# Kernel optimization log

Measured on AMD Instinct MI355X. Metric: run time of the kernel, lower is better.

## Reference

```python
import jax, jax.numpy as jnp
import numpy as np

N_NODES = 50000
N_EDGES = 640000
D = 128      # in_feats
OUT = 128    # out_feats


def setup_inputs() -> dict:
    key = jax.random.key(0)
    ks = jax.random.split(key, 8)
    feat = jax.random.normal(ks[0], (N_NODES, D), dtype=jnp.float32)
    weight = jax.random.uniform(ks[1], (N_EDGES,), dtype=jnp.float32)
    src = jax.random.randint(ks[2], (N_EDGES,), 0, N_NODES, dtype=jnp.int64)
    dst = jax.random.randint(ks[3], (N_EDGES,), 0, N_NODES, dtype=jnp.int64)
    # xavier_uniform with relu gain ~ sqrt(2)*sqrt(6/(fan_in+fan_out))
    g = np.sqrt(2.0)
    lim_pool = g * np.sqrt(6.0 / (D + D))
    lim_neigh = g * np.sqrt(6.0 / (2 * D + OUT))
    W_pool = jax.random.uniform(ks[4], (D, D), dtype=jnp.float32, minval=-lim_pool, maxval=lim_pool)
    b_pool = jnp.zeros((D,), dtype=jnp.float32)
    W_neigh = jax.random.uniform(ks[5], (OUT, 2 * D), dtype=jnp.float32, minval=-lim_neigh, maxval=lim_neigh)
    b_neigh = jnp.zeros((OUT,), dtype=jnp.float32)
    return {"feat": feat, "weight": weight, "src": src, "dst": dst,
            "W_pool": W_pool, "b_pool": b_pool, "W_neigh": W_neigh, "b_neigh": b_neigh}


def reference(feat, weight, src, dst, W_pool, b_pool, W_neigh, b_neigh):
    n = feat.shape[0]
    # fc_pool: h = feat @ W_pool.T + b_pool  -> [N, D]
    h = feat @ W_pool.T + b_pool
    # u_mul_e: per-edge message m_e = h[src_e] * w_e  -> [E, D]
    m = h[src] * weight[:, None]
    # max reduce over incoming edges (scatter-max by dst)
    neigh = jax.ops.segment_max(m, dst, num_segments=n)
    # zero-degree nodes get 0 (segment_max fills empties with -inf)
    deg = jax.ops.segment_sum(jnp.ones_like(weight), dst, num_segments=n)
    neigh = jnp.where(deg[:, None] > 0, neigh, jnp.zeros((), dtype=feat.dtype))
    # fc_neigh on concat(feat, neigh)
    rst = jnp.concatenate([feat, neigh], axis=1) @ W_neigh.T + b_neigh
    return rst
```

## Files before the change

### kernel.cpp

```cpp
#include <hip/hip_runtime.h>
#include <cstdint>
#include <cstddef>

#define N_NODES 50000
#define N_EDGES 640000
#define DF 128
#define SLOT 64

#define SC_BLOCKS 625
#define GEMM_BLOCKS 782
#define FRAG_BLOCKS 16

typedef __attribute__((ext_vector_type(8))) short bf16x8;
typedef __attribute__((ext_vector_type(4))) float f32x4;

__device__ inline unsigned short f2bf(float f) {
    unsigned int u = __float_as_uint(f);
    return (unsigned short)((u + 0x7fffu + ((u >> 16) & 1u)) >> 16);
}

__global__ __launch_bounds__(256) void k1_scatter_gemm(
    const float* __restrict__ feat,
    const float* __restrict__ W_pool,
    const float* __restrict__ W_neigh,
    const float* __restrict__ b_pool,
    const int* __restrict__ src,
    const int* __restrict__ dst,
    const float* __restrict__ w,
    unsigned short* __restrict__ featb,
    unsigned short* __restrict__ hb,
    unsigned short* __restrict__ Wn1_f,
    unsigned short* __restrict__ Wn2_f,
    int* __restrict__ cnt,
    uint2* __restrict__ edges)
{
    int bid = blockIdx.x;
    int t = threadIdx.x;
    if (bid < SC_BLOCKS) {
        int base = bid * 1024;
        #pragma unroll
        for (int k = 0; k < 4; ++k) {
            int e = base + k * 256 + t;
            int s = src[e], d = dst[e];
            float wv = w[e];
            int c = atomicAdd(&cnt[d], 1);
            if (c < SLOT) {
                uint2 r; r.x = (unsigned int)s; r.y = __float_as_uint(wv);
                edges[(size_t)d * SLOT + c] = r;
            }
        }
    } else if (bid < SC_BLOCKS + GEMM_BLOCKS) {
        __shared__ __align__(16) unsigned short wsh[16384];
        #pragma unroll
        for (int k = 0; k < 8; ++k) {
            int r8 = t * 8 + k;
            int L = r8 & 63, tt2 = (r8 >> 6) & 3, c = r8 >> 8;
            const float* srcp = W_pool + (c * 16 + (L & 15)) * 128
                                       + tt2 * 32 + (L >> 4) * 8;
            float4 a = ((const float4*)srcp)[0];
            float4 b = ((const float4*)srcp)[1];
            ushort4 lo, hi;
            lo.x = f2bf(a.x); lo.y = f2bf(a.y); lo.z = f2bf(a.z); lo.w = f2bf(a.w);
            hi.x = f2bf(b.x); hi.y = f2bf(b.y); hi.z = f2bf(b.z); hi.w = f2bf(b.w);
            ((ushort4*)(wsh + r8 * 8))[0] = lo;
            ((ushort4*)(wsh + r8 * 8))[1] = hi;
        }
        __syncthreads();

        int gwave = (bid - SC_BLOCKS) * 4 + (t >> 6);
        int m0 = gwave * 16;
        if (m0 < N_NODES) {
            int lane = t & 63;
            const int n = lane & 15, quad = lane >> 4;
            f32x4 acc[8];
            #pragma unroll
            for (int c = 0; c < 8; ++c) {
                float bv = b_pool[c * 16 + n];
                acc[c] = (f32x4){bv, bv, bv, bv};
            }
            const float* fp = feat + (size_t)(m0 + n) * DF + quad * 8;
            unsigned short* fbp = featb + (size_t)(m0 + n) * DF + quad * 8;
            #pragma unroll
            for (int tt = 0; tt < 4; ++tt) {
                float4 a = ((const float4*)(fp + tt * 32))[0];
                float4 b = ((const float4*)(fp + tt * 32))[1];
                union { bf16x8 v; ushort4 u4[2]; } af;
                af.u4[0].x = f2bf(a.x); af.u4[0].y = f2bf(a.y);
                af.u4[0].z = f2bf(a.z); af.u4[0].w = f2bf(a.w);
                af.u4[1].x = f2bf(b.x); af.u4[1].y = f2bf(b.y);
                af.u4[1].z = f2bf(b.z); af.u4[1].w = f2bf(b.w);
                *(bf16x8*)(fbp + tt * 32) = af.v;
                #pragma unroll
                for (int c = 0; c < 8; ++c) {
                    bf16x8 bfv = *(const bf16x8*)(wsh + (size_t)((c * 4 + tt) * 64 + lane) * 8);
                    acc[c] = __builtin_amdgcn_mfma_f32_16x16x32_bf16(af.v, bfv, acc[c], 0, 0, 0);
                }
            }
            #pragma unroll
            for (int c = 0; c < 8; ++c)
                #pragma unroll
                for (int r = 0; r < 4; ++r)
                    hb[(size_t)(m0 + quad * 4 + r) * DF + c * 16 + n] = f2bf(acc[c][r]);
        }
    } else {
        int g = (bid - SC_BLOCKS - GEMM_BLOCKS) * 256 + t;
        int m = g >> 11;
        int r8 = g & 2047;
        int L = r8 & 63, tt = (r8 >> 6) & 3, c = r8 >> 8;
        int o = c * 16 + (L & 15);
        int kb = tt * 32 + (L >> 4) * 8;
        const float* srcp = W_neigh + o * 256 + (m ? 128 : 0) + kb;
        unsigned short* dstp = m ? Wn2_f : Wn1_f;
        ushort4 lo, hi;
        float4 a = ((const float4*)srcp)[0];
        float4 b = ((const float4*)srcp)[1];
        lo.x = f2bf(a.x); lo.y = f2bf(a.y); lo.z = f2bf(a.z); lo.w = f2bf(a.w);
        hi.x = f2bf(b.x); hi.y = f2bf(b.y); hi.z = f2bf(b.z); hi.w = f2bf(b.w);
        ((ushort4*)(dstp + r8 * 8))[0] = lo;
        ((ushort4*)(dstp + r8 * 8))[1] = hi;
    }
}

__global__ __launch_bounds__(256) void neigh_max_kernel(
    const unsigned short* __restrict__ hb,
    const int* __restrict__ cnt,
    const uint2* __restrict__ edges,
    unsigned short* __restrict__ neighb)
{
    int gwave = (blockIdx.x * 256 + threadIdx.x) >> 6;
    if (gwave >= N_NODES) return;
    int node = __builtin_amdgcn_readfirstlane(gwave);
    int lane = threadIdx.x & 63;
    const int half = lane >> 5;
    const int q = lane & 31;

    int beg = node * SLOT;
    int dg = cnt[node]; if (dg > SLOT) dg = SLOT;
    int end = beg + dg;
    float4 acc = make_float4(-3.4e38f, -3.4e38f, -3.4e38f, -3.4e38f);

    for (int e = beg; e < end; e += 8) {
        int i1 = min(e + 1, end - 1);
        int i2 = min(e + 2, end - 1);
        int i3 = min(e + 3, end - 1);
        int i4 = min(e + 4, end - 1);
        int i5 = min(e + 5, end - 1);
        int i6 = min(e + 6, end - 1);
        int i7 = min(e + 7, end - 1);
        uint2 e0 = edges[e],  e1 = edges[i1], e2 = edges[i2], e3 = edges[i3];
        uint2 e4 = edges[i4], e5 = edges[i5], e6 = edges[i6], e7 = edges[i7];
        uint2 mA = half ? e1 : e0;
        uint2 mB = half ? e3 : e2;
        uint2 mC = half ? e5 : e4;
        uint2 mD = half ? e7 : e6;
        float wA = __uint_as_float(mA.y);
        float wB = __uint_as_float(mB.y);
        float wC = __uint_as_float(mC.y);
        float wD = __uint_as_float(mD.y);
        uint2 pA = *(const uint2*)(hb + (size_t)mA.x * DF + q * 4);
        uint2 pB = *(const uint2*)(hb + (size_t)mB.x * DF + q * 4);
        uint2 pC = *(const uint2*)(hb + (size_t)mC.x * DF + q * 4);
        uint2 pD = *(const uint2*)(hb + (size_t)mD.x * DF + q * 4);
        acc.x = fmaxf(acc.x, __uint_as_float(pA.x << 16)          * wA);
        acc.y = fmaxf(acc.y, __uint_as_float(pA.x & 0xffff0000u)  * wA);
        acc.z = fmaxf(acc.z, __uint_as_float(pA.y << 16)          * wA);
        acc.w = fmaxf(acc.w, __uint_as_float(pA.y & 0xffff0000u)  * wA);
        acc.x = fmaxf(acc.x, __uint_as_float(pB.x << 16)          * wB);
        acc.y = fmaxf(acc.y, __uint_as_float(pB.x & 0xffff0000u)  * wB);
        acc.z = fmaxf(acc.z, __uint_as_float(pB.y << 16)          * wB);
        acc.w = fmaxf(acc.w, __uint_as_float(pB.y & 0xffff0000u)  * wB);
        acc.x = fmaxf(acc.x, __uint_as_float(pC.x << 16)          * wC);
        acc.y = fmaxf(acc.y, __uint_as_float(pC.x & 0xffff0000u)  * wC);
        acc.z = fmaxf(acc.z, __uint_as_float(pC.y << 16)          * wC);
        acc.w = fmaxf(acc.w, __uint_as_float(pC.y & 0xffff0000u)  * wC);
        acc.x = fmaxf(acc.x, __uint_as_float(pD.x << 16)          * wD);
        acc.y = fmaxf(acc.y, __uint_as_float(pD.x & 0xffff0000u)  * wD);
        acc.z = fmaxf(acc.z, __uint_as_float(pD.y << 16)          * wD);
        acc.w = fmaxf(acc.w, __uint_as_float(pD.y & 0xffff0000u)  * wD);
    }

    float4 o;
    o.x = fmaxf(acc.x, __shfl_xor(acc.x, 32));
    o.y = fmaxf(acc.y, __shfl_xor(acc.y, 32));
    o.z = fmaxf(acc.z, __shfl_xor(acc.z, 32));
    o.w = fmaxf(acc.w, __shfl_xor(acc.w, 32));
    if (dg == 0) o = make_float4(0.f, 0.f, 0.f, 0.f);
    if (half == 0) {
        ushort4 ob;
        ob.x = f2bf(o.x); ob.y = f2bf(o.y); ob.z = f2bf(o.z); ob.w = f2bf(o.w);
        *(ushort4*)(neighb + (size_t)node * DF + q * 4) = ob;
    }
}

__global__ __launch_bounds__(256) void gemm_out(
    const unsigned short* __restrict__ featb,
    const unsigned short* __restrict__ neighb,
    const unsigned short* __restrict__ Wn1_f,
    const unsigned short* __restrict__ Wn2_f,
    const float* __restrict__ bias,
    float* __restrict__ out)
{
    int wave = (blockIdx.x * 256 + threadIdx.x) >> 6;
    int lane = threadIdx.x & 63;
    int m0 = wave * 16;
    if (m0 >= N_NODES) return;
    const int n = lane & 15, quad = lane >> 4;

    f32x4 acc[8];
    #pragma unroll
    for (int c = 0; c < 8; ++c) {
        float bv = bias[c * 16 + n];
        acc[c] = (f32x4){bv, bv, bv, bv};
    }

    const unsigned short* a0 = featb  + (size_t)(m0 + n) * DF + quad * 8;
    const unsigned short* a1 = neighb + (size_t)(m0 + n) * DF + quad * 8;
    #pragma unroll
    for (int t = 0; t < 4; ++t) {
        bf16x8 af = *(const bf16x8*)(a0 + t * 32);
        #pragma unroll
        for (int c = 0; c < 8; ++c) {
            bf16x8 bf = *(const bf16x8*)(Wn1_f + (size_t)((c * 4 + t) * 64 + lane) * 8);
            acc[c] = __builtin_amdgcn_mfma_f32_16x16x32_bf16(af, bf, acc[c], 0, 0, 0);
        }
    }
    #pragma unroll
    for (int t = 0; t < 4; ++t) {
        bf16x8 af = *(const bf16x8*)(a1 + t * 32);
        #pragma unroll
        for (int c = 0; c < 8; ++c) {
            bf16x8 bf = *(const bf16x8*)(Wn2_f + (size_t)((c * 4 + t) * 64 + lane) * 8);
            acc[c] = __builtin_amdgcn_mfma_f32_16x16x32_bf16(af, bf, acc[c], 0, 0, 0);
        }
    }

    #pragma unroll
    for (int c = 0; c < 8; ++c)
        #pragma unroll
        for (int r = 0; r < 4; ++r)
            out[(size_t)(m0 + quad * 4 + r) * DF + c * 16 + n] = acc[c][r];
}

extern "C" void kernel_launch(void* const* d_in, const int* in_sizes, int n_in,
                              void* d_out, int out_size, void* d_ws, size_t ws_size,
                              hipStream_t stream) {
    const float* feat    = (const float*)d_in[0];
    const float* weight  = (const float*)d_in[1];
    const int*   src     = (const int*)d_in[2];
    const int*   dst     = (const int*)d_in[3];
    const float* W_pool  = (const float*)d_in[4];
    const float* b_pool  = (const float*)d_in[5];
    const float* W_neigh = (const float*)d_in[6];
    const float* b_neigh = (const float*)d_in[7];
    float* out = (float*)d_out;

    char* ws = (char*)d_ws;
    unsigned short* featb  = (unsigned short*)(ws);
    unsigned short* hb     = (unsigned short*)(ws + 12800000);
    unsigned short* Wn1_f  = (unsigned short*)(ws + 25600000);
    unsigned short* Wn2_f  = (unsigned short*)(ws + 25632768);
    int*   cnt       = (int*)  (ws + 25665536);
    uint2* edges     = (uint2*)(ws + 25865536);
    unsigned short* neighb = (unsigned short*)(ws + 51465536);

    hipMemsetAsync(cnt, 0, N_NODES * sizeof(int), stream);

    const int K1_BLOCKS = SC_BLOCKS + GEMM_BLOCKS + FRAG_BLOCKS;
    k1_scatter_gemm<<<K1_BLOCKS, 256, 0, stream>>>(
        feat, W_pool, W_neigh, b_pool, src, dst, weight,
        featb, hb, Wn1_f, Wn2_f, cnt, edges);

    neigh_max_kernel<<<(N_NODES + 3) / 4, 256, 0, stream>>>(
        hb, cnt, edges, neighb);

    gemm_out<<<782, 256, 0, stream>>>(
        featb, neighb, Wn1_f, Wn2_f, b_neigh, out);
}
```

Measured before the change: 171.1 us.

## Fuse neighbor max-reduction with output GEMM via shared memory

Merges the per-node max aggregation and the final fc_neigh GEMM into one 1024-thread kernel. Each block handles 16 nodes: 16 waves each reduce one node's neighbors into a swizzled LDS tile, while 8 of them also compute the feat half of the GEMM, then after a barrier those 8 waves do the neigh half, one 16-column slice each. This removes the neighb round trip through global memory and a kernel launch. The scatter phase now uses one edge per thread across more blocks, and the W_pool staging loop is re-indexed for coalesced access. The cost is a block-wide barrier and only half the waves active in the GEMM tail.

```diff
diff --git a/kernel.cpp b/kernel.cpp
--- a/kernel.cpp
+++ b/kernel.cpp
@@ -7,8 +7,8 @@
 #define DF 128
 #define SLOT 64
 
-#define SC_BLOCKS 625
-#define GEMM_BLOCKS 782
+#define SC_BLOCKS 2500
+#define GEMMB 782
 #define FRAG_BLOCKS 16
 
 typedef __attribute__((ext_vector_type(8))) short bf16x8;
@@ -19,7 +19,7 @@
     return (unsigned short)((u + 0x7fffu + ((u >> 16) & 1u)) >> 16);
 }
 
-__global__ __launch_bounds__(256) void k1_scatter_gemm(
+__global__ __launch_bounds__(256) void d1_scatter_gemm(
     const float* __restrict__ feat,
     const float* __restrict__ W_pool,
     const float* __restrict__ W_neigh,
@@ -37,23 +37,19 @@
     int bid = blockIdx.x;
     int t = threadIdx.x;
     if (bid < SC_BLOCKS) {
-        int base = bid * 1024;
-        #pragma unroll
-        for (int k = 0; k < 4; ++k) {
-            int e = base + k * 256 + t;
-            int s = src[e], d = dst[e];
-            float wv = w[e];
-            int c = atomicAdd(&cnt[d], 1);
-            if (c < SLOT) {
-                uint2 r; r.x = (unsigned int)s; r.y = __float_as_uint(wv);
-                edges[(size_t)d * SLOT + c] = r;
-            }
-        }
-    } else if (bid < SC_BLOCKS + GEMM_BLOCKS) {
+        int e = bid * 256 + t;
+        int s = src[e], d = dst[e];
+        float wv = w[e];
+        int c = atomicAdd(&cnt[d], 1);
+        if (c < SLOT) {
+            uint2 r; r.x = (unsigned int)s; r.y = __float_as_uint(wv);
+            edges[(size_t)d * SLOT + c] = r;
+        }
+    } else if (bid < SC_BLOCKS + GEMMB) {
         __shared__ __align__(16) unsigned short wsh[16384];
         #pragma unroll
         for (int k = 0; k < 8; ++k) {
-            int r8 = t * 8 + k;
+            int r8 = k * 256 + t;
             int L = r8 & 63, tt2 = (r8 >> 6) & 3, c = r8 >> 8;
             const float* srcp = W_pool + (c * 16 + (L & 15)) * 128
                                        + tt2 * 32 + (L >> 4) * 8;
@@ -103,7 +99,7 @@
                     hb[(size_t)(m0 + quad * 4 + r) * DF + c * 16 + n] = f2bf(acc[c][r]);
         }
     } else {
-        int g = (bid - SC_BLOCKS - GEMM_BLOCKS) * 256 + t;
+        int g = (bid - SC_BLOCKS - GEMMB) * 256 + t;
         int m = g >> 11;
         int r8 = g & 2047;
         int L = r8 & 63, tt = (r8 >> 6) & 3, c = r8 >> 8;
@@ -121,23 +117,28 @@
     }
 }
 
-__global__ __launch_bounds__(256) void neigh_max_kernel(
+__global__ __launch_bounds__(1024) void fused_max_out(
+    const unsigned short* __restrict__ featb,
     const unsigned short* __restrict__ hb,
     const int* __restrict__ cnt,
     const uint2* __restrict__ edges,
-    unsigned short* __restrict__ neighb)
+    const unsigned short* __restrict__ Wn1_f,
+    const unsigned short* __restrict__ Wn2_f,
+    const float* __restrict__ bias,
+    float* __restrict__ out)
 {
-    int gwave = (blockIdx.x * 256 + threadIdx.x) >> 6;
-    if (gwave >= N_NODES) return;
-    int node = __builtin_amdgcn_readfirstlane(gwave);
-    int lane = threadIdx.x & 63;
+    __shared__ __align__(16) unsigned short nsh[16 * DF];
+    const int t = threadIdx.x;
+    const int lane = t & 63;
+    const int wid = t >> 6;
+    const int m0 = blockIdx.x * 16;
     const int half = lane >> 5;
     const int q = lane & 31;
 
-    int beg = node * SLOT;
+    const int node = __builtin_amdgcn_readfirstlane(m0 + wid);
     int dg = cnt[node]; if (dg > SLOT) dg = SLOT;
-    int end = beg + dg;
-    float4 acc = make_float4(-3.4e38f, -3.4e38f, -3.4e38f, -3.4e38f);
+    int beg = node * SLOT, end = beg + dg;
+    float4 mx = make_float4(-3.4e38f, -3.4e38f, -3.4e38f, -3.4e38f);
 
     for (int e = beg; e < end; e += 8) {
         int i1 = min(e + 1, end - 1);
@@ -161,84 +162,67 @@
         uint2 pB = *(const uint2*)(hb + (size_t)mB.x * DF + q * 4);
         uint2 pC = *(const uint2*)(hb + (size_t)mC.x * DF + q * 4);
         uint2 pD = *(const uint2*)(hb + (size_t)mD.x * DF + q * 4);
-        acc.x = fmaxf(acc.x, __uint_as_float(pA.x << 16)          * wA);
-        acc.y = fmaxf(acc.y, __uint_as_float(pA.x & 0xffff0000u)  * wA);
-        acc.z = fmaxf(acc.z, __uint_as_float(pA.y << 16)          * wA);
-        acc.w = fmaxf(acc.w, __uint_as_float(pA.y & 0xffff0000u)  * wA);
-        acc.x = fmaxf(acc.x, __uint_as_float(pB.x << 16)          * wB);
-        acc.y = fmaxf(acc.y, __uint_as_float(pB.x & 0xffff0000u)  * wB);
-        acc.z = fmaxf(acc.z, __uint_as_float(pB.y << 16)          * wB);
-        acc.w = fmaxf(acc.w, __uint_as_float(pB.y & 0xffff0000u)  * wB);
-        acc.x = fmaxf(acc.x, __uint_as_float(pC.x << 16)          * wC);
-        acc.y = fmaxf(acc.y, __uint_as_float(pC.x & 0xffff0000u)  * wC);
-        acc.z = fmaxf(acc.z, __uint_as_float(pC.y << 16)          * wC);
-        acc.w = fmaxf(acc.w, __uint_as_float(pC.y & 0xffff0000u)  * wC);
-        acc.x = fmaxf(acc.x, __uint_as_float(pD.x << 16)          * wD);
-        acc.y = fmaxf(acc.y, __uint_as_float(pD.x & 0xffff0000u)  * wD);
-        acc.z = fmaxf(acc.z, __uint_as_float(pD.y << 16)          * wD);
-        acc.w = fmaxf(acc.w, __uint_as_float(pD.y & 0xffff0000u)  * wD);
+        mx.x = fmaxf(mx.x, __uint_as_float(pA.x << 16)          * wA);
+        mx.y = fmaxf(mx.y, __uint_as_float(pA.x & 0xffff0000u)  * wA);
+        mx.z = fmaxf(mx.z, __uint_as_float(pA.y << 16)          * wA);
+        mx.w = fmaxf(mx.w, __uint_as_float(pA.y & 0xffff0000u)  * wA);
+        mx.x = fmaxf(mx.x, __uint_as_float(pB.x << 16)          * wB);
+        mx.y = fmaxf(mx.y, __uint_as_float(pB.x & 0xffff0000u)  * wB);
+        mx.z = fmaxf(mx.z, __uint_as_float(pB.y << 16)          * wB);
+        mx.w = fmaxf(mx.w, __uint_as_float(pB.y & 0xffff0000u)  * wB);
+        mx.x = fmaxf(mx.x, __uint_as_float(pC.x << 16)          * wC);
+        mx.y = fmaxf(mx.y, __uint_as_float(pC.x & 0xffff0000u)  * wC);
+        mx.z = fmaxf(mx.z, __uint_as_float(pC.y << 16)          * wC);
+        mx.w = fmaxf(mx.w, __uint_as_float(pC.y & 0xffff0000u)  * wC);
+        mx.x = fmaxf(mx.x, __uint_as_float(pD.x << 16)          * wD);
+        mx.y = fmaxf(mx.y, __uint_as_float(pD.x & 0xffff0000u)  * wD);
+        mx.z = fmaxf(mx.z, __uint_as_float(pD.y << 16)          * wD);
+        mx.w = fmaxf(mx.w, __uint_as_float(pD.y & 0xffff0000u)  * wD);
     }
 
     float4 o;
-    o.x = fmaxf(acc.x, __shfl_xor(acc.x, 32));
-    o.y = fmaxf(acc.y, __shfl_xor(acc.y, 32));
-    o.z = fmaxf(acc.z, __shfl_xor(acc.z, 32));
-    o.w = fmaxf(acc.w, __shfl_xor(acc.w, 32));
+    o.x = fmaxf(mx.x, __shfl_xor(mx.x, 32));
+    o.y = fmaxf(mx.y, __shfl_xor(mx.y, 32));
+    o.z = fmaxf(mx.z, __shfl_xor(mx.z, 32));
+    o.w = fmaxf(mx.w, __shfl_xor(mx.w, 32));
     if (dg == 0) o = make_float4(0.f, 0.f, 0.f, 0.f);
     if (half == 0) {
         ushort4 ob;
         ob.x = f2bf(o.x); ob.y = f2bf(o.y); ob.z = f2bf(o.z); ob.w = f2bf(o.w);
-        *(ushort4*)(neighb + (size_t)node * DF + q * 4) = ob;
-    }
-}
-
-__global__ __launch_bounds__(256) void gemm_out(
-    const unsigned short* __restrict__ featb,
-    const unsigned short* __restrict__ neighb,
-    const unsigned short* __restrict__ Wn1_f,
-    const unsigned short* __restrict__ Wn2_f,
-    const float* __restrict__ bias,
-    float* __restrict__ out)
-{
-    int wave = (blockIdx.x * 256 + threadIdx.x) >> 6;
-    int lane = threadIdx.x & 63;
-    int m0 = wave * 16;
-    if (m0 >= N_NODES) return;
+        int boff = wid * 256 + ((q * 8) ^ ((wid & 7) << 4));
+        *(ushort4*)((char*)nsh + boff) = ob;
+    }
+
     const int n = lane & 15, quad = lane >> 4;
-
-    f32x4 acc[8];
+    f32x4 acc;
+    if (wid < 8) {
+        const int c = wid;
+        float bv = bias[c * 16 + n];
+        acc = (f32x4){bv, bv, bv, bv};
+        const unsigned short* a0 = featb + (size_t)(m0 + n) * DF + quad * 8;
+        #pragma unroll
+        for (int tt = 0; tt < 4; ++tt) {
+            bf16x8 af = *(const bf16x8*)(a0 + tt * 32);
+            bf16x8 bfv = *(const bf16x8*)(Wn1_f + (size_t)((c * 4 + tt) * 64 + lane) * 8);
+            acc = __builtin_amdgcn_mfma_f32_16x16x32_bf16(af, bfv, acc, 0, 0, 0);
+        }
+    }
+
+    __syncthreads();
+    if (wid >= 8) return;
+
+    const int c = wid;
     #pragma unroll
-    for (int c = 0; c < 8; ++c) {
-        float bv = bias[c * 16 + n];
-        acc[c] = (f32x4){bv, bv, bv, bv};
-    }
-
-    const unsigned short* a0 = featb  + (size_t)(m0 + n) * DF + quad * 8;
-    const unsigned short* a1 = neighb + (size_t)(m0 + n) * DF + quad * 8;
+    for (int tt = 0; tt < 4; ++tt) {
+        int boff = (quad * 16 + tt * 64) ^ ((n & 7) << 4);
+        bf16x8 af = *(const bf16x8*)((const char*)nsh + n * 256 + boff);
+        bf16x8 bfv = *(const bf16x8*)(Wn2_f + (size_t)((c * 4 + tt) * 64 + lane) * 8);
+        acc = __builtin_amdgcn_mfma_f32_16x16x32_bf16(af, bfv, acc, 0, 0, 0);
+    }
+
     #pragma unroll
-    for (int t = 0; t < 4; ++t) {
-        bf16x8 af = *(const bf16x8*)(a0 + t * 32);
-        #pragma unroll
-        for (int c = 0; c < 8; ++c) {
-            bf16x8 bf = *(const bf16x8*)(Wn1_f + (size_t)((c * 4 + t) * 64 + lane) * 8);
-            acc[c] = __builtin_amdgcn_mfma_f32_16x16x32_bf16(af, bf, acc[c], 0, 0, 0);
-        }
-    }
-    #pragma unroll
-    for (int t = 0; t < 4; ++t) {
-        bf16x8 af = *(const bf16x8*)(a1 + t * 32);
-        #pragma unroll
-        for (int c = 0; c < 8; ++c) {
-            bf16x8 bf = *(const bf16x8*)(Wn2_f + (size_t)((c * 4 + t) * 64 + lane) * 8);
-            acc[c] = __builtin_amdgcn_mfma_f32_16x16x32_bf16(af, bf, acc[c], 0, 0, 0);
-        }
-    }
-
-    #pragma unroll
-    for (int c = 0; c < 8; ++c)
-        #pragma unroll
-        for (int r = 0; r < 4; ++r)
-            out[(size_t)(m0 + quad * 4 + r) * DF + c * 16 + n] = acc[c][r];
+    for (int r = 0; r < 4; ++r)
+        out[(size_t)(m0 + quad * 4 + r) * DF + c * 16 + n] = acc[r];
 }
 
 extern "C" void kernel_launch(void* const* d_in, const int* in_sizes, int n_in,
@@ -261,18 +245,14 @@
     unsigned short* Wn2_f  = (unsigned short*)(ws + 25632768);
     int*   cnt       = (int*)  (ws + 25665536);
     uint2* edges     = (uint2*)(ws + 25865536);
-    unsigned short* neighb = (unsigned short*)(ws + 51465536);
 
     hipMemsetAsync(cnt, 0, N_NODES * sizeof(int), stream);
 
-    const int K1_BLOCKS = SC_BLOCKS + GEMM_BLOCKS + FRAG_BLOCKS;
-    k1_scatter_gemm<<<K1_BLOCKS, 256, 0, stream>>>(
+    const int D1_BLOCKS = SC_BLOCKS + GEMMB + FRAG_BLOCKS;
+    d1_scatter_gemm<<<D1_BLOCKS, 256, 0, stream>>>(
         feat, W_pool, W_neigh, b_pool, src, dst, weight,
         featb, hb, Wn1_f, Wn2_f, cnt, edges);
 
-    neigh_max_kernel<<<(N_NODES + 3) / 4, 256, 0, stream>>>(
-        hb, cnt, edges, neighb);
-
-    gemm_out<<<782, 256, 0, stream>>>(
-        featb, neighb, Wn1_f, Wn2_f, b_neigh, out);
-}
+    fused_max_out<<<N_NODES / 16, 1024, 0, stream>>>(
+        featb, hb, cnt, edges, Wn1_f, Wn2_f, b_neigh, out);
+}
```

Result: slower. 177.9 us (+4.0%).
